# Kernel optimization log

Measured on AMD Instinct MI355X. Metric: run time of the kernel, lower is better.

## Reference

```python
import jax, jax.numpy as jnp
import numpy as np

NX = 8        # state dim
NU = 8        # control dim (== NX, required by original Fx assignment)
N = 64        # horizon
BATCH = 2048
M = N * NU    # condensed QP size = 512
MAX_ITER = 100
STEP = 0.01
U_MIN, U_MAX = -1.0, 1.0


def _build_buffers():
    rng = np.random.default_rng(0)
    A = rng.standard_normal((NX, NX))
    A /= 1.05 * np.max(np.abs(np.linalg.eigvals(A)))  # stable dynamics
    Bm = 0.1 * rng.standard_normal((NX, NU))
    Q = np.eye(NX)
    R = 0.1 * np.eye(NU)
    Qf = np.eye(NX)
    # Phi[k] = A^k
    Phi = np.zeros((N + 1, NX, NX))
    Phi[0] = np.eye(NX)
    for i in range(N):
        Phi[i + 1] = A @ Phi[i]
    # Gamma[i][:, j*NU:(j+1)*NU] = A^{i-1-j} B  (x_i = A^i x0 + Gamma_i u)
    Gamma = np.zeros((N + 1, NX, M))
    for i in range(1, N + 1):
        for j in range(i):
            Gamma[i, :, j * NU:(j + 1) * NU] = Phi[i - 1 - j] @ Bm
    # Condensed Hessian H_bar = sum_i Gamma_i^T Q Gamma_i + blockdiag(R) + reg
    H = np.zeros((M, M))
    for i in range(1, N):
        H += Gamma[i].T @ Q @ Gamma[i]
    H += Gamma[N].T @ Qf @ Gamma[N]
    H += np.kron(np.eye(N), R)
    H += 1e-6 * np.eye(M)
    return (jnp.asarray(H, jnp.float32), jnp.asarray(Phi, jnp.float32),
            jnp.asarray(Q, jnp.float32))


def setup_inputs() -> dict:
    key = jax.random.key(0)
    k1, k2 = jax.random.split(key)
    x0 = jax.random.normal(k1, (BATCH, NX), dtype=jnp.float32)
    xref = jax.random.normal(k2, (BATCH, N + 1, NX), dtype=jnp.float32)
    H, Phi, Q = _build_buffers()
    return {"x0": x0, "xref": xref, "H": H, "Phi": Phi, "Q": Q}


def reference(x0, xref, H, Phi, Q):
    # Linear term f: Fx_k = -2 * Phi[k] @ Q @ (xref_k - xref_0)   [B, N, NX]
    dx = xref[:, :N] - xref[:, :1]                       # [B, N, NX]
    Fx = -2.0 * jnp.einsum('kij,jl,bkl->bki', Phi[:N], Q, dx)
    f = Fx.reshape(xref.shape[0], M)                     # [B, M]

    # Projected gradient descent QP solve: 100 iterations of
    #   u <- clip(u - step*(H u + f), u_min, u_max)
    def step(u, _):
        grad = u @ H.T + f                               # [B, M]
        u_new = jnp.clip(u - STEP * grad, U_MIN, U_MAX)
        return u_new, None

    u0 = jnp.zeros_like(f)
    u, _ = jax.lax.scan(step, u0, None, length=MAX_ITER)
    return u  # full optimal control sequence [B, N*NU]
```

## Files before the change

### kernel.cpp

```cpp
#include <hip/hip_runtime.h>


typedef unsigned short u16t;
typedef __attribute__((ext_vector_type(8))) short short8;
typedef __attribute__((ext_vector_type(4))) float floatx4;

#define HLDS_BYTES (128 * 520 * 2)
#define UBF_BYTES  (16 * 520 * 2)
#define DYN_LDS    (HLDS_BYTES + UBF_BYTES)

__device__ __forceinline__ u16t f32_to_bf16(float x) {
    unsigned int u = __builtin_bit_cast(unsigned int, x);
    u = (u + 0x7FFFu + ((u >> 16) & 1u)) >> 16;
    return (u16t)u;
}

__global__ void convert_H_bf16(const float* __restrict__ H, u16t* __restrict__ Hb) {
    int idx = blockIdx.x * 256 + threadIdx.x;
    Hb[idx] = f32_to_bf16(H[idx]);
}

#define MFMA(a, b, c) __builtin_amdgcn_mfma_f32_16x16x32_bf16((a), (b), (c), 0, 0, 0)

__global__ __launch_bounds__(512, 2)
void pgd_kernel5(const float* __restrict__ xref,
                 const float* __restrict__ H,
                 const u16t*  __restrict__ Hb,
                 const float* __restrict__ Phi,
                 const float* __restrict__ Q,
                 float* __restrict__ out)
{
    extern __shared__ __align__(16) char smem[];
    u16t* Hlds = (u16t*)smem;
    u16t (*u_bf)[520] = (u16t(*)[520])(smem + HLDS_BYTES);

    const int tid  = threadIdx.x;
    const int lane = tid & 63;
    const int w    = tid >> 6;
    const int quad = lane >> 4;
    const int lcol = lane & 15;
    const int b0   = blockIdx.x * 16;
    const int colbase = w * 64;

    for (int e = tid; e < 8192; e += 512) {
        int r = e >> 6, c = e & 63;
        *(short8*)&Hlds[r * 520 + c * 8] =
            *(const short8*)&Hb[(long)((r >> 4) * 64 + 32 + (r & 15)) * 512 + c * 8];
    }
    {
        u16t* ub = &u_bf[0][0];
        for (int e = tid; e < 8320; e += 512) ub[e] = 0;
    }

    short8 hfragA[2][16];
    #pragma unroll
    for (int t = 0; t < 2; ++t) {
        const float* hrow = H + (long)(colbase + t * 16 + lcol) * 512;
        #pragma unroll
        for (int ks = 0; ks < 16; ++ks) {
            const float* hp = hrow + ks * 32 + quad * 8;
            short8 fr;
            #pragma unroll
            for (int j = 0; j < 8; ++j) fr[j] = (short)f32_to_bf16(hp[j]);
            hfragA[t][ks] = fr;
        }
    }
    short8 frag3[8];
    {
        const float* hrow = H + (long)(colbase + 48 + lcol) * 512;
        #pragma unroll
        for (int ks = 0; ks < 8; ++ks) {
            const float* hp = hrow + ks * 32 + quad * 8;
            short8 fr;
            #pragma unroll
            for (int j = 0; j < 8; ++j) fr[j] = (short)f32_to_bf16(hp[j]);
            frag3[ks] = fr;
        }
    }

    float f_reg[4][4], u_reg[4][4];
    #pragma unroll
    for (int T = 0; T < 4; ++T) {
        int c = colbase + T * 16 + lcol;
        int k = c >> 3, i = c & 7;
        #pragma unroll
        for (int r = 0; r < 4; ++r) {
            int m = quad * 4 + r;
            const float* xr = xref + (long)(b0 + m) * 520;
            float s = 0.f;
            #pragma unroll
            for (int j = 0; j < 8; ++j) {
                float z = 0.f;
                #pragma unroll
                for (int l = 0; l < 8; ++l) z += Q[j * 8 + l] * (xr[k * 8 + l] - xr[l]);
                s += Phi[k * 64 + i * 8 + j] * z;
            }
            f_reg[T][r] = -2.0f * s;
            u_reg[T][r] = 0.0f;
        }
    }
    __syncthreads();

    const u16t* hb3 = Hb + (long)(colbase + 48 + lcol) * 512;
    const u16t* h2  = Hlds + (w * 16 + lcol) * 520;

    short8 sb0 = *(const short8*)&hb3[8 * 32 + quad * 8];
    short8 sb1 = *(const short8*)&hb3[9 * 32 + quad * 8];

    for (int it = 0; it < 100; ++it) {
        floatx4 acc[4];
        #pragma unroll
        for (int T = 0; T < 4; ++T) acc[T] = (floatx4){0.f, 0.f, 0.f, 0.f};

        #pragma unroll
        for (int ks = 0; ks < 8; ++ks) {
            short8 a  = *(const short8*)&u_bf[lcol][ks * 32 + quad * 8];
            short8 b2 = *(const short8*)&h2[ks * 32 + quad * 8];
            acc[0] = MFMA(a, hfragA[0][ks], acc[0]);
            acc[1] = MFMA(a, hfragA[1][ks], acc[1]);
            acc[2] = MFMA(a, b2, acc[2]);
            acc[3] = MFMA(a, frag3[ks], acc[3]);
        }
        #pragma unroll
        for (int ks = 8; ks < 16; ++ks) {
            short8 a  = *(const short8*)&u_bf[lcol][ks * 32 + quad * 8];
            short8 b2 = *(const short8*)&h2[ks * 32 + quad * 8];
            short8 b3 = sb0;
            sb0 = sb1;
            sb1 = *(const short8*)&hb3[(8 + ((ks - 6) & 7)) * 32 + quad * 8];
            acc[0] = MFMA(a, hfragA[0][ks], acc[0]);
            acc[1] = MFMA(a, hfragA[1][ks], acc[1]);
            acc[2] = MFMA(a, b2, acc[2]);
            acc[3] = MFMA(a, b3, acc[3]);
        }

        #pragma unroll
        for (int T = 0; T < 4; ++T)
            #pragma unroll
            for (int r = 0; r < 4; ++r) {
                float g  = acc[T][r] + f_reg[T][r];
                float un = u_reg[T][r] - 0.01f * g;
                un = fminf(1.0f, fmaxf(-1.0f, un));
                u_reg[T][r] = un;
            }

        __syncthreads();
        #pragma unroll
        for (int T = 0; T < 4; ++T) {
            int c = colbase + T * 16 + lcol;
            #pragma unroll
            for (int r = 0; r < 4; ++r)
                u_bf[quad * 4 + r][c] = f32_to_bf16(u_reg[T][r]);
        }
        __syncthreads();
    }

    #pragma unroll
    for (int T = 0; T < 4; ++T) {
        int c = colbase + T * 16 + lcol;
        #pragma unroll
        for (int r = 0; r < 4; ++r)
            out[(long)(b0 + quad * 4 + r) * 512 + c] = u_reg[T][r];
    }
}

extern "C" void kernel_launch(void* const* d_in, const int* in_sizes, int n_in,
                              void* d_out, int out_size, void* d_ws, size_t ws_size,
                              hipStream_t stream) {
    const float* xref = (const float*)d_in[1];
    const float* H    = (const float*)d_in[2];
    const float* Phi  = (const float*)d_in[3];
    const float* Q    = (const float*)d_in[4];
    u16t* Hb = (u16t*)d_ws;

    (void)hipFuncSetAttribute((const void*)pgd_kernel5,
                              hipFuncAttributeMaxDynamicSharedMemorySize, DYN_LDS);

    convert_H_bf16<<<1024, 256, 0, stream>>>(H, Hb);
    pgd_kernel5<<<128, 512, DYN_LDS, stream>>>(xref, H, Hb, Phi, Q, (float*)d_out);
}
```

Measured before the change: 254.8 us.

## Double-buffer bf16 u in LDS and stream upper half of H tile 2 from global

The bf16 iterate buffer is double-buffered, so each iteration writes the new u into the alternate buffer and needs only one barrier instead of two. To make room in LDS, only the first 256 columns of the third H tile are kept in shared memory. The remaining half is streamed from global/L2 through a two-deep register prefetch, like the fourth tile already was. The f computation is moved before the H fragment loads. This trades a barrier and a serial store phase per iteration for more global load traffic in the inner loop.

```diff
diff --git a/kernel.cpp b/kernel.cpp
--- a/kernel.cpp
+++ b/kernel.cpp
@@ -5,9 +5,9 @@
 typedef __attribute__((ext_vector_type(8))) short short8;
 typedef __attribute__((ext_vector_type(4))) float floatx4;
 
-#define HLDS_BYTES (128 * 520 * 2)
+#define HLDS_BYTES (128 * 264 * 2)
 #define UBF_BYTES  (16 * 520 * 2)
-#define DYN_LDS    (HLDS_BYTES + UBF_BYTES)
+#define DYN_LDS    (HLDS_BYTES + 2 * UBF_BYTES)
 
 __device__ __forceinline__ u16t f32_to_bf16(float x) {
     unsigned int u = __builtin_bit_cast(unsigned int, x);
@@ -23,7 +23,7 @@
 #define MFMA(a, b, c) __builtin_amdgcn_mfma_f32_16x16x32_bf16((a), (b), (c), 0, 0, 0)
 
 __global__ __launch_bounds__(512, 2)
-void pgd_kernel5(const float* __restrict__ xref,
+void pgd_kernel6(const float* __restrict__ xref,
                  const float* __restrict__ H,
                  const u16t*  __restrict__ Hb,
                  const float* __restrict__ Phi,
@@ -32,7 +32,8 @@
 {
     extern __shared__ __align__(16) char smem[];
     u16t* Hlds = (u16t*)smem;
-    u16t (*u_bf)[520] = (u16t(*)[520])(smem + HLDS_BYTES);
+    u16t (*ubuf0)[520] = (u16t(*)[520])(smem + HLDS_BYTES);
+    u16t (*ubuf1)[520] = (u16t(*)[520])(smem + HLDS_BYTES + UBF_BYTES);
 
     const int tid  = threadIdx.x;
     const int lane = tid & 63;
@@ -42,14 +43,36 @@
     const int b0   = blockIdx.x * 16;
     const int colbase = w * 64;
 
-    for (int e = tid; e < 8192; e += 512) {
-        int r = e >> 6, c = e & 63;
-        *(short8*)&Hlds[r * 520 + c * 8] =
+    for (int e = tid; e < 4096; e += 512) {
+        int r = e >> 5, c = e & 31;
+        *(short8*)&Hlds[r * 264 + c * 8] =
             *(const short8*)&Hb[(long)((r >> 4) * 64 + 32 + (r & 15)) * 512 + c * 8];
     }
     {
-        u16t* ub = &u_bf[0][0];
-        for (int e = tid; e < 8320; e += 512) ub[e] = 0;
+        u16t* ub = (u16t*)(smem + HLDS_BYTES);
+        for (int e = tid; e < 16640; e += 512) ub[e] = 0;
+    }
+
+    float f_reg[4][4], u_reg[4][4];
+    #pragma unroll
+    for (int T = 0; T < 4; ++T) {
+        int c = colbase + T * 16 + lcol;
+        int k = c >> 3, i = c & 7;
+        #pragma unroll
+        for (int r = 0; r < 4; ++r) {
+            int m = quad * 4 + r;
+            const float* xr = xref + (long)(b0 + m) * 520;
+            float s = 0.f;
+            #pragma unroll
+            for (int j = 0; j < 8; ++j) {
+                float z = 0.f;
+                #pragma unroll
+                for (int l = 0; l < 8; ++l) z += Q[j * 8 + l] * (xr[k * 8 + l] - xr[l]);
+                s += Phi[k * 64 + i * 8 + j] * z;
+            }
+            f_reg[T][r] = -2.0f * s;
+            u_reg[T][r] = 0.0f;
+        }
     }
 
     short8 hfragA[2][16];
@@ -77,35 +100,19 @@
             frag3[ks] = fr;
         }
     }
-
-    float f_reg[4][4], u_reg[4][4];
-    #pragma unroll
-    for (int T = 0; T < 4; ++T) {
-        int c = colbase + T * 16 + lcol;
-        int k = c >> 3, i = c & 7;
-        #pragma unroll
-        for (int r = 0; r < 4; ++r) {
-            int m = quad * 4 + r;
-            const float* xr = xref + (long)(b0 + m) * 520;
-            float s = 0.f;
-            #pragma unroll
-            for (int j = 0; j < 8; ++j) {
-                float z = 0.f;
-                #pragma unroll
-                for (int l = 0; l < 8; ++l) z += Q[j * 8 + l] * (xr[k * 8 + l] - xr[l]);
-                s += Phi[k * 64 + i * 8 + j] * z;
-            }
-            f_reg[T][r] = -2.0f * s;
-            u_reg[T][r] = 0.0f;
-        }
-    }
     __syncthreads();
 
-    const u16t* hb3 = Hb + (long)(colbase + 48 + lcol) * 512;
-    const u16t* h2  = Hlds + (w * 16 + lcol) * 520;
+    const u16t* hb2s = Hb + (long)(colbase + 32 + lcol) * 512;
+    const u16t* hb3  = Hb + (long)(colbase + 48 + lcol) * 512;
+    const u16t* h2   = Hlds + (w * 16 + lcol) * 264;
 
+    short8 tb0 = *(const short8*)&hb2s[8 * 32 + quad * 8];
+    short8 tb1 = *(const short8*)&hb2s[9 * 32 + quad * 8];
     short8 sb0 = *(const short8*)&hb3[8 * 32 + quad * 8];
     short8 sb1 = *(const short8*)&hb3[9 * 32 + quad * 8];
+
+    u16t (*ub_r)[520] = ubuf0;
+    u16t (*ub_w)[520] = ubuf1;
 
     for (int it = 0; it < 100; ++it) {
         floatx4 acc[4];
@@ -114,7 +121,7 @@
 
         #pragma unroll
         for (int ks = 0; ks < 8; ++ks) {
-            short8 a  = *(const short8*)&u_bf[lcol][ks * 32 + quad * 8];
+            short8 a  = *(const short8*)&ub_r[lcol][ks * 32 + quad * 8];
             short8 b2 = *(const short8*)&h2[ks * 32 + quad * 8];
             acc[0] = MFMA(a, hfragA[0][ks], acc[0]);
             acc[1] = MFMA(a, hfragA[1][ks], acc[1]);
@@ -123,8 +130,10 @@
         }
         #pragma unroll
         for (int ks = 8; ks < 16; ++ks) {
-            short8 a  = *(const short8*)&u_bf[lcol][ks * 32 + quad * 8];
-            short8 b2 = *(const short8*)&h2[ks * 32 + quad * 8];
+            short8 a  = *(const short8*)&ub_r[lcol][ks * 32 + quad * 8];
+            short8 b2 = tb0;
+            tb0 = tb1;
+            tb1 = *(const short8*)&hb2s[(8 + ((ks - 6) & 7)) * 32 + quad * 8];
             short8 b3 = sb0;
             sb0 = sb1;
             sb1 = *(const short8*)&hb3[(8 + ((ks - 6) & 7)) * 32 + quad * 8];
@@ -135,24 +144,20 @@
         }
 
         #pragma unroll
-        for (int T = 0; T < 4; ++T)
+        for (int T = 0; T < 4; ++T) {
+            int c = colbase + T * 16 + lcol;
             #pragma unroll
             for (int r = 0; r < 4; ++r) {
                 float g  = acc[T][r] + f_reg[T][r];
                 float un = u_reg[T][r] - 0.01f * g;
                 un = fminf(1.0f, fmaxf(-1.0f, un));
                 u_reg[T][r] = un;
+                ub_w[quad * 4 + r][c] = f32_to_bf16(un);
             }
+        }
 
         __syncthreads();
-        #pragma unroll
-        for (int T = 0; T < 4; ++T) {
-            int c = colbase + T * 16 + lcol;
-            #pragma unroll
-            for (int r = 0; r < 4; ++r)
-                u_bf[quad * 4 + r][c] = f32_to_bf16(u_reg[T][r]);
-        }
-        __syncthreads();
+        u16t (*tmp)[520] = ub_r; ub_r = ub_w; ub_w = tmp;
     }
 
     #pragma unroll
@@ -173,9 +178,9 @@
     const float* Q    = (const float*)d_in[4];
     u16t* Hb = (u16t*)d_ws;
 
-    (void)hipFuncSetAttribute((const void*)pgd_kernel5,
+    (void)hipFuncSetAttribute((const void*)pgd_kernel6,
                               hipFuncAttributeMaxDynamicSharedMemorySize, DYN_LDS);
 
     convert_H_bf16<<<1024, 256, 0, stream>>>(H, Hb);
-    pgd_kernel5<<<128, 512, DYN_LDS, stream>>>(xref, H, Hb, Phi, Q, (float*)d_out);
+    pgd_kernel6<<<128, 512, DYN_LDS, stream>>>(xref, H, Hb, Phi, Q, (float*)d_out);
 }
```

New measurement: 437.3 us. 1.72x slower.

## Double-buffer u in LDS with XOR swizzle to drop one barrier per iteration

Applied to the files above, without the earlier changes.

Replaces the padded u and H LDS layouts with an XOR-swizzled 512-wide layout to avoid bank conflicts without padding. The u tile is now double-buffered, so each iteration writes the new bf16 u to the other buffer right after the clip and needs only one __syncthreads instead of two. The global prefetch of H fragments is also deepened from two to four registers, and the f computation moves earlier. This costs extra LDS and registers and adds swizzle index arithmetic.

```diff
diff --git a/kernel.cpp b/kernel.cpp
--- a/kernel.cpp
+++ b/kernel.cpp
@@ -5,9 +5,9 @@
 typedef __attribute__((ext_vector_type(8))) short short8;
 typedef __attribute__((ext_vector_type(4))) float floatx4;
 
-#define HLDS_BYTES (128 * 520 * 2)
-#define UBF_BYTES  (16 * 520 * 2)
-#define DYN_LDS    (HLDS_BYTES + UBF_BYTES)
+#define HLDS_BYTES (128 * 512 * 2)
+#define UBF_BYTES  (16 * 512 * 2)
+#define DYN_LDS    (HLDS_BYTES + 2 * UBF_BYTES)
 
 __device__ __forceinline__ u16t f32_to_bf16(float x) {
     unsigned int u = __builtin_bit_cast(unsigned int, x);
@@ -23,7 +23,7 @@
 #define MFMA(a, b, c) __builtin_amdgcn_mfma_f32_16x16x32_bf16((a), (b), (c), 0, 0, 0)
 
 __global__ __launch_bounds__(512, 2)
-void pgd_kernel5(const float* __restrict__ xref,
+void pgd_kernel7(const float* __restrict__ xref,
                  const float* __restrict__ H,
                  const u16t*  __restrict__ Hb,
                  const float* __restrict__ Phi,
@@ -31,8 +31,9 @@
                  float* __restrict__ out)
 {
     extern __shared__ __align__(16) char smem[];
-    u16t* Hlds = (u16t*)smem;
-    u16t (*u_bf)[520] = (u16t(*)[520])(smem + HLDS_BYTES);
+    u16t* Hlds  = (u16t*)smem;
+    u16t* ubuf0 = (u16t*)(smem + HLDS_BYTES);
+    u16t* ubuf1 = (u16t*)(smem + HLDS_BYTES + UBF_BYTES);
 
     const int tid  = threadIdx.x;
     const int lane = tid & 63;
@@ -43,13 +44,36 @@
     const int colbase = w * 64;
 
     for (int e = tid; e < 8192; e += 512) {
-        int r = e >> 6, c = e & 63;
-        *(short8*)&Hlds[r * 520 + c * 8] =
-            *(const short8*)&Hb[(long)((r >> 4) * 64 + 32 + (r & 15)) * 512 + c * 8];
+        int r = e >> 6, g = e & 63;
+        *(short8*)&Hlds[r * 512 + ((g ^ (r & 7)) << 3)] =
+            *(const short8*)&Hb[(long)((r >> 4) * 64 + 32 + (r & 15)) * 512 + g * 8];
     }
     {
-        u16t* ub = &u_bf[0][0];
-        for (int e = tid; e < 8320; e += 512) ub[e] = 0;
+        short8 z8 = (short8){0,0,0,0,0,0,0,0};
+        short8* ub = (short8*)ubuf0;
+        for (int e = tid; e < 2048; e += 512) ub[e] = z8;
+    }
+
+    float f_reg[4][4], u_reg[4][4];
+    #pragma unroll
+    for (int T = 0; T < 4; ++T) {
+        int c = colbase + T * 16 + lcol;
+        int k = c >> 3, i = c & 7;
+        #pragma unroll
+        for (int r = 0; r < 4; ++r) {
+            int m = quad * 4 + r;
+            const float* xr = xref + (long)(b0 + m) * 520;
+            float s = 0.f;
+            #pragma unroll
+            for (int j = 0; j < 8; ++j) {
+                float z = 0.f;
+                #pragma unroll
+                for (int l = 0; l < 8; ++l) z += Q[j * 8 + l] * (xr[k * 8 + l] - xr[l]);
+                s += Phi[k * 64 + i * 8 + j] * z;
+            }
+            f_reg[T][r] = -2.0f * s;
+            u_reg[T][r] = 0.0f;
+        }
     }
 
     short8 hfragA[2][16];
@@ -77,45 +101,30 @@
             frag3[ks] = fr;
         }
     }
-
-    float f_reg[4][4], u_reg[4][4];
-    #pragma unroll
-    for (int T = 0; T < 4; ++T) {
-        int c = colbase + T * 16 + lcol;
-        int k = c >> 3, i = c & 7;
-        #pragma unroll
-        for (int r = 0; r < 4; ++r) {
-            int m = quad * 4 + r;
-            const float* xr = xref + (long)(b0 + m) * 520;
-            float s = 0.f;
-            #pragma unroll
-            for (int j = 0; j < 8; ++j) {
-                float z = 0.f;
-                #pragma unroll
-                for (int l = 0; l < 8; ++l) z += Q[j * 8 + l] * (xr[k * 8 + l] - xr[l]);
-                s += Phi[k * 64 + i * 8 + j] * z;
-            }
-            f_reg[T][r] = -2.0f * s;
-            u_reg[T][r] = 0.0f;
-        }
-    }
     __syncthreads();
 
     const u16t* hb3 = Hb + (long)(colbase + 48 + lcol) * 512;
-    const u16t* h2  = Hlds + (w * 16 + lcol) * 520;
+    short8 sb0 = *(const short8*)&hb3[ 8 * 32 + quad * 8];
+    short8 sb1 = *(const short8*)&hb3[ 9 * 32 + quad * 8];
+    short8 sb2 = *(const short8*)&hb3[10 * 32 + quad * 8];
+    short8 sb3 = *(const short8*)&hb3[11 * 32 + quad * 8];
 
-    short8 sb0 = *(const short8*)&hb3[8 * 32 + quad * 8];
-    short8 sb1 = *(const short8*)&hb3[9 * 32 + quad * 8];
+    const int  swz = (lcol & 7) << 3;
+    const u16t* h2 = &Hlds[(w * 16 + lcol) * 512];
+    u16t* ub_r = ubuf0;
+    u16t* ub_w = ubuf1;
 
     for (int it = 0; it < 100; ++it) {
+        const u16t* ar = &ub_r[lcol * 512];
         floatx4 acc[4];
         #pragma unroll
         for (int T = 0; T < 4; ++T) acc[T] = (floatx4){0.f, 0.f, 0.f, 0.f};
 
         #pragma unroll
         for (int ks = 0; ks < 8; ++ks) {
-            short8 a  = *(const short8*)&u_bf[lcol][ks * 32 + quad * 8];
-            short8 b2 = *(const short8*)&h2[ks * 32 + quad * 8];
+            int goff = (((ks * 4 + quad) << 3) ^ swz);
+            short8 a  = *(const short8*)&ar[goff];
+            short8 b2 = *(const short8*)&h2[goff];
             acc[0] = MFMA(a, hfragA[0][ks], acc[0]);
             acc[1] = MFMA(a, hfragA[1][ks], acc[1]);
             acc[2] = MFMA(a, b2, acc[2]);
@@ -123,11 +132,12 @@
         }
         #pragma unroll
         for (int ks = 8; ks < 16; ++ks) {
-            short8 a  = *(const short8*)&u_bf[lcol][ks * 32 + quad * 8];
-            short8 b2 = *(const short8*)&h2[ks * 32 + quad * 8];
+            int goff = (((ks * 4 + quad) << 3) ^ swz);
+            short8 a  = *(const short8*)&ar[goff];
+            short8 b2 = *(const short8*)&h2[goff];
             short8 b3 = sb0;
-            sb0 = sb1;
-            sb1 = *(const short8*)&hb3[(8 + ((ks - 6) & 7)) * 32 + quad * 8];
+            sb0 = sb1; sb1 = sb2; sb2 = sb3;
+            sb3 = *(const short8*)&hb3[(8 + ((ks - 4) & 7)) * 32 + quad * 8];
             acc[0] = MFMA(a, hfragA[0][ks], acc[0]);
             acc[1] = MFMA(a, hfragA[1][ks], acc[1]);
             acc[2] = MFMA(a, b2, acc[2]);
@@ -135,24 +145,21 @@
         }
 
         #pragma unroll
-        for (int T = 0; T < 4; ++T)
+        for (int T = 0; T < 4; ++T) {
+            int c = colbase + T * 16 + lcol;
             #pragma unroll
             for (int r = 0; r < 4; ++r) {
                 float g  = acc[T][r] + f_reg[T][r];
                 float un = u_reg[T][r] - 0.01f * g;
                 un = fminf(1.0f, fmaxf(-1.0f, un));
                 u_reg[T][r] = un;
+                int m = quad * 4 + r;
+                ub_w[m * 512 + (((c >> 3) ^ (m & 7)) << 3) + (c & 7)] = f32_to_bf16(un);
             }
+        }
 
         __syncthreads();
-        #pragma unroll
-        for (int T = 0; T < 4; ++T) {
-            int c = colbase + T * 16 + lcol;
-            #pragma unroll
-            for (int r = 0; r < 4; ++r)
-                u_bf[quad * 4 + r][c] = f32_to_bf16(u_reg[T][r]);
-        }
-        __syncthreads();
+        u16t* tmp = ub_r; ub_r = ub_w; ub_w = tmp;
     }
 
     #pragma unroll
@@ -173,9 +180,9 @@
     const float* Q    = (const float*)d_in[4];
     u16t* Hb = (u16t*)d_ws;
 
-    (void)hipFuncSetAttribute((const void*)pgd_kernel5,
+    (void)hipFuncSetAttribute((const void*)pgd_kernel7,
                               hipFuncAttributeMaxDynamicSharedMemorySize, DYN_LDS);
 
     convert_H_bf16<<<1024, 256, 0, stream>>>(H, Hb);
-    pgd_kernel5<<<128, 512, DYN_LDS, stream>>>(xref, H, Hb, Phi, Q, (float*)d_out);
+    pgd_kernel7<<<128, 512, DYN_LDS, stream>>>(xref, H, Hb, Phi, Q, (float*)d_out);
 }
```

Measured after the change: 516.2 us. +102.6%, slower.
